# Kernel tuning notes

Hardware: AMD Instinct MI355X
Metric: run time of the kernel (lower is better)

## Reference

```python
import jax, jax.numpy as jnp
import numpy as np
from jax import lax

IN_C, OUT_C, K, Z_DIM, STRIDE = 128, 128, 3, 256, 1


def setup_inputs() -> dict:
    key = jax.random.key(0)
    k1, k2, k3, k4, k5 = jax.random.split(key, 5)
    B, H, W = 16, 64, 64
    x = jax.random.normal(k1, (B, IN_C, H, W), dtype=jnp.float32)
    z = jax.random.normal(k2, (B, Z_DIM), dtype=jnp.float32)
    # base conv weight, He-style init as in the torch module
    base_weight = jax.random.normal(k3, (OUT_C, IN_C, K, K), dtype=jnp.float32) * (2.0 / (IN_C * K * K)) ** 0.5
    # delta_weight_head: nn.Linear(z_dim, out_c*in_c*k*k) -> weight [out_dim, z_dim], bias [out_dim]
    out_dim = OUT_C * IN_C * K * K
    lim = 1.0 / np.sqrt(Z_DIM)
    head_w = jax.random.uniform(k4, (out_dim, Z_DIM), dtype=jnp.float32, minval=-lim, maxval=lim)
    head_b = jax.random.uniform(k5, (out_dim,), dtype=jnp.float32, minval=-lim, maxval=lim)
    return {"x": x, "z": z, "base_weight": base_weight, "head_w": head_w, "head_b": head_b}


def reference(x, z, base_weight, head_w, head_b):
    B = x.shape[0]
    # per-sample weight deltas: [B, out_c*in_c*k*k] -> [B, out_c, in_c, k, k]
    delta_w = (z @ head_w.T + head_b).reshape(B, OUT_C, IN_C, K, K)
    w = base_weight[None] + delta_w  # [B, out_c, in_c, k, k]
    pad = K // 2

    def conv_one(xb, wb):
        # xb: [in_c, H, W], wb: [out_c, in_c, k, k]
        return lax.conv_general_dilated(
            xb[None], wb, window_strides=(STRIDE, STRIDE),
            padding=[(pad, pad), (pad, pad)],
            dimension_numbers=("NCHW", "OIHW", "NCHW"))[0]

    out = jax.vmap(conv_one)(x, w)  # [B, out_c, H_out, W_out]
    return out
```

## Files before the change

### kernel.cpp

```cpp
#include <hip/hip_runtime.h>
#include <hip/hip_bf16.h>
#include <cstdint>
#include <cstddef>

typedef _Float16 f16;
typedef _Float16 f16x8 __attribute__((ext_vector_type(8)));
typedef _Float16 f16x4 __attribute__((ext_vector_type(4)));
typedef float f32x4 __attribute__((ext_vector_type(4)));

#define BATCH 16
#define INC   128
#define OUTC  128
#define HH    64
#define WW    64
#define HP    66
#define WP    66
#define ZDIM  256

#define XP_ELEMS (16ull * HP * WP * INC)
#define WA_ELEMS (16ull * 9 * OUTC * INC)

__global__ __launch_bounds__(256) void zero_xp(f16* __restrict__ xp) {
    unsigned i = blockIdx.x * 256 + threadIdx.x;
    unsigned b = i / 4160;
    unsigned j = i - b * 4160;
    unsigned row, wc, ic8;
    if (j < 2112) {
        row = (j < 1056) ? 0u : 65u;
        unsigned jj = (j < 1056) ? j : j - 1056;
        wc  = jj >> 4;
        ic8 = jj & 15;
    } else {
        unsigned j2 = j - 2112;
        row = 1 + (j2 >> 5);
        unsigned k = j2 & 31;
        wc  = (k < 16) ? 0u : 65u;
        ic8 = k & 15;
    }
    uint4 zv = {0u, 0u, 0u, 0u};
    *(uint4*)(xp + (((size_t)b * HP + row) * WP + wc) * INC + ic8 * 8) = zv;
}

__global__ __launch_bounds__(256) void xprep(const float* __restrict__ x,
                                             f16* __restrict__ xp) {
    int blk = blockIdx.x;
    int icC = blk & 3;
    int h   = (blk >> 2) & 63;
    int b   = blk >> 8;
    int ic0 = icC * 32;
    int tid = threadIdx.x;

    __shared__ float tile[32 * 65];

    {
        int i = tid >> 3;
        int j = tid & 7;
        const float4* src = (const float4*)(x + (((size_t)b * INC + ic0 + i) * HH + h) * WW) + j * 2;
        float4 v0 = src[0];
        float4 v1 = src[1];
        float* tp = tile + i * 65 + j * 8;
        tp[0] = v0.x; tp[1] = v0.y; tp[2] = v0.z; tp[3] = v0.w;
        tp[4] = v1.x; tp[5] = v1.y; tp[6] = v1.z; tp[7] = v1.w;
    }
    __syncthreads();
    {
        int w = tid >> 2;
        int q = tid & 3;
        f16 o8[8];
#pragma unroll
        for (int jj = 0; jj < 8; ++jj)
            o8[jj] = (f16)tile[(q * 8 + jj) * 65 + w];
        f16* dst = xp + (((size_t)b * HP + (h + 1)) * WP + (w + 1)) * INC + ic0 + q * 8;
        *(uint4*)dst = *(uint4*)o8;
    }
}

__device__ inline f16x8 cvt8(float4 a, float4 b) {
    f16x8 r;
    r[0] = (f16)a.x; r[1] = (f16)a.y; r[2] = (f16)a.z; r[3] = (f16)a.w;
    r[4] = (f16)b.x; r[5] = (f16)b.y; r[6] = (f16)b.z; r[7] = (f16)b.w;
    return r;
}

__global__ __launch_bounds__(256) void wgen(const float* __restrict__ z,
                                            const float* __restrict__ base_w,
                                            const float* __restrict__ head_w,
                                            const float* __restrict__ head_b,
                                            f16* __restrict__ wA) {
    int tid  = threadIdx.x;
    int lane = tid & 63;
    int wv   = tid >> 6;
    int r16  = lane & 15;
    int quad = lane >> 4;
    int tile = blockIdx.x * 4 + wv;
    int icb  = tile & 7;
    int oc   = (tile >> 3) & 127;
    int r    = tile >> 10;
    int base = (oc * 128 + icb * 16) * 9 + r;
    int myrow = base + 9 * r16;

    const float4* zrow = (const float4*)(z + (size_t)r16 * ZDIM);
    f16x8 bfr[8];
#pragma unroll
    for (int s = 0; s < 8; ++s)
        bfr[s] = cvt8(zrow[s * 8 + quad * 2], zrow[s * 8 + quad * 2 + 1]);

    const float4* hw = (const float4*)(head_w + (size_t)myrow * ZDIM);
    float4 a[3][2];
    a[0][0] = hw[quad * 2];     a[0][1] = hw[quad * 2 + 1];
    a[1][0] = hw[8 + quad * 2]; a[1][1] = hw[8 + quad * 2 + 1];
    f32x4 acc = {0.f, 0.f, 0.f, 0.f};
#pragma unroll
    for (int s = 0; s < 8; ++s) {
        if (s + 2 < 8) {
            a[(s + 2) % 3][0] = hw[(s + 2) * 8 + quad * 2];
            a[(s + 2) % 3][1] = hw[(s + 2) * 8 + quad * 2 + 1];
        }
        acc = __builtin_amdgcn_mfma_f32_16x16x32_f16(
            cvt8(a[s % 3][0], a[s % 3][1]), bfr[s], acc, 0, 0, 0);
    }

    f16x4 ov;
    int icl = quad * 4;
#pragma unroll
    for (int reg = 0; reg < 4; ++reg) {
        int o = base + 9 * (icl + reg);
        ov[reg] = (f16)(base_w[o] + head_b[o] + acc[reg]);
    }
    size_t idx = (((size_t)r16 * 9 + r) * OUTC + oc) * INC + icb * 16 + icl;
    *(f16x4*)(wA + idx) = ov;
}

__global__ __launch_bounds__(256) void conv(const f16* __restrict__ xp,
                                            const f16* __restrict__ wA,
                                            float* __restrict__ out) {
    int blk = blockIdx.x;
    int b  = blk >> 5;
    int pt = blk & 31;
    int h0 = pt * 2;

    int tid   = threadIdx.x;
    int lane  = tid & 63;
    int wv    = tid >> 6;
    int ocHalf = wv & 1;
    int pHalf  = wv >> 1;
    int m0    = ocHalf * 64;
    int row16 = lane & 15;
    int quad  = lane >> 4;

    __shared__ __align__(16) f16 ws3[3 * 128 * 40];
    __shared__ __align__(16) f16 xs[4 * 66 * 40];

    f32x4 acc[4][4];
#pragma unroll
    for (int mt = 0; mt < 4; ++mt)
#pragma unroll
        for (int nt = 0; nt < 4; ++nt)
            acc[mt][nt] = f32x4{0.f, 0.f, 0.f, 0.f};

    for (int c = 0; c < 4; ++c) {
        int ic0 = c * 32;
#pragma unroll
        for (int kh = 0; kh < 3; ++kh) {
            __syncthreads();
#pragma unroll
            for (int i = 0; i < 6; ++i) {
                int idx  = tid + i * 256;
                int seg  = idx >> 2;
                int part = idx & 3;
                int kw = seg >> 7;
                int oc = seg & 127;
                const uint4* src = (const uint4*)(wA +
                    ((((size_t)b * 9 + kh * 3 + kw) * OUTC + oc) * INC + ic0)) + part;
                *(uint4*)(ws3 + (kw * 128 + oc) * 40 + part * 8) = *src;
            }
            if (kh == 0) {
                for (int idx = tid; idx < 1056; idx += 256) {
                    int seg  = idx >> 2;
                    int part = idx & 3;
                    int row  = seg / 66;
                    int wc   = seg - row * 66;
                    const uint4* src = (const uint4*)(xp +
                        (((size_t)b * HP + h0 + row) * WP + wc) * INC + ic0) + part;
                    *(uint4*)(xs + (row * 66 + wc) * 40 + part * 8) = *src;
                }
            }
            __syncthreads();
#pragma unroll
            for (int kw = 0; kw < 3; ++kw) {
                f16x8 afr[4], bfr[4];
#pragma unroll
                for (int mt = 0; mt < 4; ++mt)
                    afr[mt] = *(const f16x8*)(ws3 + ((kw * 128 + m0 + mt * 16 + row16) * 40 + quad * 8));
#pragma unroll
                for (int nt = 0; nt < 4; ++nt)
                    bfr[nt] = *(const f16x8*)(xs + (((kh + pHalf) * 66 + nt * 16 + row16 + kw) * 40 + quad * 8));
#pragma unroll
                for (int mt = 0; mt < 4; ++mt)
#pragma unroll
                    for (int nt = 0; nt < 4; ++nt)
                        acc[mt][nt] = __builtin_amdgcn_mfma_f32_16x16x32_f16(
                            afr[mt], bfr[nt], acc[mt][nt], 0, 0, 0);
            }
        }
    }

    int hrow = h0 + pHalf;
#pragma unroll
    for (int mt = 0; mt < 4; ++mt)
#pragma unroll
        for (int nt = 0; nt < 4; ++nt) {
            int wc = nt * 16 + row16;
#pragma unroll
            for (int reg = 0; reg < 4; ++reg) {
                int oc = m0 + mt * 16 + quad * 4 + reg;
                out[(((size_t)b * OUTC + oc) * HH + hrow) * WW + wc] = acc[mt][nt][reg];
            }
        }
}

extern "C" void kernel_launch(void* const* d_in, const int* in_sizes, int n_in,
                              void* d_out, int out_size, void* d_ws, size_t ws_size,
                              hipStream_t stream) {
    const float* x      = (const float*)d_in[0];
    const float* z      = (const float*)d_in[1];
    const float* base_w = (const float*)d_in[2];
    const float* head_w = (const float*)d_in[3];
    const float* head_b = (const float*)d_in[4];
    float* out = (float*)d_out;

    f16* xp = (f16*)d_ws;
    f16* wAp = xp + XP_ELEMS;

    zero_xp<<<260, 256, 0, stream>>>(xp);
    xprep  <<<16 * 64 * 4, 256, 0, stream>>>(x, xp);
    wgen   <<<(OUTC * INC * 9) / 64, 256, 0, stream>>>(z, base_w, head_w,
                                                       head_b, wAp);
    conv   <<<16 * 32, 256, 0, stream>>>(xp, wAp, out);
}
```

Measured before the change: 288.8 us.

## Merge prep kernels and double-buffer conv weights via direct global-to-LDS loads

Folds the zero-padding, input transpose and weight-generation kernels into one launch, which removes two kernel launch gaps. In the conv kernel, weight tiles are double-buffered and fetched with global_load_lds so each next tile streams in while MFMAs run on the current one. Blocks are remapped so that batches are interleaved across XCDs, and the LDS row pitch drops from 40 to 32 halves. The unpadded pitch risks LDS bank conflicts, and the two-buffer scheme raises LDS use per block.

```diff
diff --git a/kernel.cpp b/kernel.cpp
--- a/kernel.cpp
+++ b/kernel.cpp
@@ -1,5 +1,4 @@
 #include <hip/hip_runtime.h>
-#include <hip/hip_bf16.h>
 #include <cstdint>
 #include <cstddef>
 
@@ -20,136 +19,143 @@
 #define XP_ELEMS (16ull * HP * WP * INC)
 #define WA_ELEMS (16ull * 9 * OUTC * INC)
 
-__global__ __launch_bounds__(256) void zero_xp(f16* __restrict__ xp) {
-    unsigned i = blockIdx.x * 256 + threadIdx.x;
-    unsigned b = i / 4160;
-    unsigned j = i - b * 4160;
-    unsigned row, wc, ic8;
-    if (j < 2112) {
-        row = (j < 1056) ? 0u : 65u;
-        unsigned jj = (j < 1056) ? j : j - 1056;
-        wc  = jj >> 4;
-        ic8 = jj & 15;
-    } else {
-        unsigned j2 = j - 2112;
-        row = 1 + (j2 >> 5);
-        unsigned k = j2 & 31;
-        wc  = (k < 16) ? 0u : 65u;
-        ic8 = k & 15;
-    }
-    uint4 zv = {0u, 0u, 0u, 0u};
-    *(uint4*)(xp + (((size_t)b * HP + row) * WP + wc) * INC + ic8 * 8) = zv;
-}
-
-__global__ __launch_bounds__(256) void xprep(const float* __restrict__ x,
-                                             f16* __restrict__ xp) {
-    int blk = blockIdx.x;
-    int icC = blk & 3;
-    int h   = (blk >> 2) & 63;
-    int b   = blk >> 8;
-    int ic0 = icC * 32;
-    int tid = threadIdx.x;
-
-    __shared__ float tile[32 * 65];
-
-    {
-        int i = tid >> 3;
-        int j = tid & 7;
-        const float4* src = (const float4*)(x + (((size_t)b * INC + ic0 + i) * HH + h) * WW) + j * 2;
-        float4 v0 = src[0];
-        float4 v1 = src[1];
-        float* tp = tile + i * 65 + j * 8;
-        tp[0] = v0.x; tp[1] = v0.y; tp[2] = v0.z; tp[3] = v0.w;
-        tp[4] = v1.x; tp[5] = v1.y; tp[6] = v1.z; tp[7] = v1.w;
-    }
-    __syncthreads();
-    {
-        int w = tid >> 2;
-        int q = tid & 3;
-        f16 o8[8];
-#pragma unroll
-        for (int jj = 0; jj < 8; ++jj)
-            o8[jj] = (f16)tile[(q * 8 + jj) * 65 + w];
-        f16* dst = xp + (((size_t)b * HP + (h + 1)) * WP + (w + 1)) * INC + ic0 + q * 8;
-        *(uint4*)dst = *(uint4*)o8;
-    }
-}
-
-__device__ inline f16x8 cvt8(float4 a, float4 b) {
+#define GLOAD16(g, l)                                                     \
+    __builtin_amdgcn_global_load_lds(                                     \
+        (const __attribute__((address_space(1))) void*)(g),               \
+        (__attribute__((address_space(3))) void*)(l), 16, 0, 0)
+
+__device__ __forceinline__ f16x8 cvt8(float4 a, float4 b) {
     f16x8 r;
     r[0] = (f16)a.x; r[1] = (f16)a.y; r[2] = (f16)a.z; r[3] = (f16)a.w;
     r[4] = (f16)b.x; r[5] = (f16)b.y; r[6] = (f16)b.z; r[7] = (f16)b.w;
     return r;
 }
 
-__global__ __launch_bounds__(256) void wgen(const float* __restrict__ z,
+__global__ __launch_bounds__(256) void prep(const float* __restrict__ x,
+                                            const float* __restrict__ z,
                                             const float* __restrict__ base_w,
                                             const float* __restrict__ head_w,
                                             const float* __restrict__ head_b,
+                                            f16* __restrict__ xp,
                                             f16* __restrict__ wA) {
-    int tid  = threadIdx.x;
-    int lane = tid & 63;
-    int wv   = tid >> 6;
-    int r16  = lane & 15;
-    int quad = lane >> 4;
-    int tile = blockIdx.x * 4 + wv;
-    int icb  = tile & 7;
-    int oc   = (tile >> 3) & 127;
-    int r    = tile >> 10;
-    int base = (oc * 128 + icb * 16) * 9 + r;
-    int myrow = base + 9 * r16;
-
-    const float4* zrow = (const float4*)(z + (size_t)r16 * ZDIM);
-    f16x8 bfr[8];
-#pragma unroll
-    for (int s = 0; s < 8; ++s)
-        bfr[s] = cvt8(zrow[s * 8 + quad * 2], zrow[s * 8 + quad * 2 + 1]);
-
-    const float4* hw = (const float4*)(head_w + (size_t)myrow * ZDIM);
-    float4 a[3][2];
-    a[0][0] = hw[quad * 2];     a[0][1] = hw[quad * 2 + 1];
-    a[1][0] = hw[8 + quad * 2]; a[1][1] = hw[8 + quad * 2 + 1];
-    f32x4 acc = {0.f, 0.f, 0.f, 0.f};
-#pragma unroll
-    for (int s = 0; s < 8; ++s) {
-        if (s + 2 < 8) {
-            a[(s + 2) % 3][0] = hw[(s + 2) * 8 + quad * 2];
-            a[(s + 2) % 3][1] = hw[(s + 2) * 8 + quad * 2 + 1];
-        }
-        acc = __builtin_amdgcn_mfma_f32_16x16x32_f16(
-            cvt8(a[s % 3][0], a[s % 3][1]), bfr[s], acc, 0, 0, 0);
+    __shared__ float tile[32 * 65];
+    int blk = blockIdx.x;
+    int tid = threadIdx.x;
+
+    if (blk < 2304) {
+        int lane = tid & 63;
+        int wv   = tid >> 6;
+        int r16  = lane & 15;
+        int quad = lane >> 4;
+        int tl   = blk * 4 + wv;
+        int icb  = tl & 7;
+        int oc   = (tl >> 3) & 127;
+        int r    = tl >> 10;
+        int base = (oc * 128 + icb * 16) * 9 + r;
+        int myrow = base + 9 * r16;
+
+        const float4* zrow = (const float4*)(z + (size_t)r16 * ZDIM);
+        f16x8 bfr[8];
+#pragma unroll
+        for (int s = 0; s < 8; ++s)
+            bfr[s] = cvt8(zrow[s * 8 + quad * 2], zrow[s * 8 + quad * 2 + 1]);
+
+        const float4* hw = (const float4*)(head_w + (size_t)myrow * ZDIM);
+        float4 a[3][2];
+        a[0][0] = hw[quad * 2];     a[0][1] = hw[quad * 2 + 1];
+        a[1][0] = hw[8 + quad * 2]; a[1][1] = hw[8 + quad * 2 + 1];
+        f32x4 acc = {0.f, 0.f, 0.f, 0.f};
+#pragma unroll
+        for (int s = 0; s < 8; ++s) {
+            if (s + 2 < 8) {
+                a[(s + 2) % 3][0] = hw[(s + 2) * 8 + quad * 2];
+                a[(s + 2) % 3][1] = hw[(s + 2) * 8 + quad * 2 + 1];
+            }
+            acc = __builtin_amdgcn_mfma_f32_16x16x32_f16(
+                cvt8(a[s % 3][0], a[s % 3][1]), bfr[s], acc, 0, 0, 0);
+        }
+
+        f16x4 ov;
+        int icl = quad * 4;
+#pragma unroll
+        for (int reg = 0; reg < 4; ++reg) {
+            int o = base + 9 * (icl + reg);
+            ov[reg] = (f16)(base_w[o] + head_b[o] + acc[reg]);
+        }
+        size_t idx = (((size_t)r16 * 9 + r) * OUTC + oc) * INC + icb * 16 + icl;
+        *(f16x4*)(wA + idx) = ov;
+
+    } else if (blk < 6400) {
+        int xb  = blk - 2304;
+        int icC = xb & 3;
+        int h   = (xb >> 2) & 63;
+        int b   = xb >> 8;
+        int ic0 = icC * 32;
+        {
+            int i = tid >> 3;
+            int j = tid & 7;
+            const float4* src = (const float4*)(x + (((size_t)b * INC + ic0 + i) * HH + h) * WW) + j * 2;
+            float4 v0 = src[0];
+            float4 v1 = src[1];
+            float* tp = tile + i * 65 + j * 8;
+            tp[0] = v0.x; tp[1] = v0.y; tp[2] = v0.z; tp[3] = v0.w;
+            tp[4] = v1.x; tp[5] = v1.y; tp[6] = v1.z; tp[7] = v1.w;
+        }
+        __syncthreads();
+        {
+            int w = tid >> 2;
+            int q = tid & 3;
+            f16 o8[8];
+#pragma unroll
+            for (int jj = 0; jj < 8; ++jj)
+                o8[jj] = (f16)tile[(q * 8 + jj) * 65 + w];
+            f16* dst = xp + (((size_t)b * HP + (h + 1)) * WP + (w + 1)) * INC + ic0 + q * 8;
+            *(uint4*)dst = *(uint4*)o8;
+        }
+
+    } else {
+        unsigned i = (unsigned)(blk - 6400) * 256u + (unsigned)tid;
+        unsigned b = i / 4160;
+        unsigned j = i - b * 4160;
+        unsigned row, wc, ic8;
+        if (j < 2112) {
+            row = (j < 1056) ? 0u : 65u;
+            unsigned jj = (j < 1056) ? j : j - 1056;
+            wc  = jj >> 4;
+            ic8 = jj & 15;
+        } else {
+            unsigned j2 = j - 2112;
+            row = 1 + (j2 >> 5);
+            unsigned k = j2 & 31;
+            wc  = (k < 16) ? 0u : 65u;
+            ic8 = k & 15;
+        }
+        uint4 zv = {0u, 0u, 0u, 0u};
+        *(uint4*)(xp + (((size_t)b * HP + row) * WP + wc) * INC + ic8 * 8) = zv;
     }
-
-    f16x4 ov;
-    int icl = quad * 4;
-#pragma unroll
-    for (int reg = 0; reg < 4; ++reg) {
-        int o = base + 9 * (icl + reg);
-        ov[reg] = (f16)(base_w[o] + head_b[o] + acc[reg]);
-    }
-    size_t idx = (((size_t)r16 * 9 + r) * OUTC + oc) * INC + icb * 16 + icl;
-    *(f16x4*)(wA + idx) = ov;
 }
 
 __global__ __launch_bounds__(256) void conv(const f16* __restrict__ xp,
                                             const f16* __restrict__ wA,
                                             float* __restrict__ out) {
-    int blk = blockIdx.x;
+    int blk0 = blockIdx.x;
+    int blk  = (blk0 & 7) * 64 + (blk0 >> 3);
     int b  = blk >> 5;
     int pt = blk & 31;
     int h0 = pt * 2;
 
-    int tid   = threadIdx.x;
-    int lane  = tid & 63;
-    int wv    = tid >> 6;
+    int tid    = threadIdx.x;
+    int lane   = tid & 63;
+    int wv     = tid >> 6;
     int ocHalf = wv & 1;
     int pHalf  = wv >> 1;
-    int m0    = ocHalf * 64;
-    int row16 = lane & 15;
-    int quad  = lane >> 4;
-
-    __shared__ __align__(16) f16 ws3[3 * 128 * 40];
-    __shared__ __align__(16) f16 xs[4 * 66 * 40];
+    int m0     = ocHalf * 64;
+    int row16  = lane & 15;
+    int quad   = lane >> 4;
+
+    __shared__ __align__(16) f16 ws0[3 * 128 * 32];
+    __shared__ __align__(16) f16 ws1[3 * 128 * 32];
+    __shared__ __align__(16) f16 xs [4 * 66 * 32];
 
     f32x4 acc[4][4];
 #pragma unroll
@@ -158,49 +164,71 @@
         for (int nt = 0; nt < 4; ++nt)
             acc[mt][nt] = f32x4{0.f, 0.f, 0.f, 0.f};
 
-    for (int c = 0; c < 4; ++c) {
-        int ic0 = c * 32;
-#pragma unroll
-        for (int kh = 0; kh < 3; ++kh) {
-            __syncthreads();
-#pragma unroll
-            for (int i = 0; i < 6; ++i) {
-                int idx  = tid + i * 256;
+    auto stage_w = [&](f16* wb, int c, int kh) {
+#pragma unroll
+        for (int i = 0; i < 6; ++i) {
+            int idx  = tid + i * 256;
+            int kw   = idx >> 9;
+            int oc   = (idx >> 2) & 127;
+            int part = idx & 3;
+            const f16* src = wA +
+                ((((size_t)b * 9 + kh * 3 + kw) * OUTC + oc) * INC + c * 32 + part * 8);
+            GLOAD16(src, wb + (size_t)idx * 8);
+        }
+    };
+    auto stage_x = [&](int c) {
+#pragma unroll
+        for (int i = 0; i < 5; ++i) {
+            int idx = tid + i * 256;
+            if (idx < 1056) {
                 int seg  = idx >> 2;
                 int part = idx & 3;
-                int kw = seg >> 7;
-                int oc = seg & 127;
-                const uint4* src = (const uint4*)(wA +
-                    ((((size_t)b * 9 + kh * 3 + kw) * OUTC + oc) * INC + ic0)) + part;
-                *(uint4*)(ws3 + (kw * 128 + oc) * 40 + part * 8) = *src;
-            }
-            if (kh == 0) {
-                for (int idx = tid; idx < 1056; idx += 256) {
-                    int seg  = idx >> 2;
-                    int part = idx & 3;
-                    int row  = seg / 66;
-                    int wc   = seg - row * 66;
-                    const uint4* src = (const uint4*)(xp +
-                        (((size_t)b * HP + h0 + row) * WP + wc) * INC + ic0) + part;
-                    *(uint4*)(xs + (row * 66 + wc) * 40 + part * 8) = *src;
-                }
-            }
-            __syncthreads();
+                int row  = seg / 66;
+                int wc   = seg - row * 66;
+                const f16* src = xp +
+                    ((((size_t)b * HP + h0 + row) * WP + wc) * INC + c * 32 + part * 8);
+                GLOAD16(src, xs + (size_t)idx * 8);
+            }
+        }
+    };
+
+    stage_x(0);
+    stage_w(ws0, 0, 0);
+    __syncthreads();
+
+#pragma unroll
+    for (int c = 0; c < 4; ++c) {
+#pragma unroll
+        for (int kh = 0; kh < 3; ++kh) {
+            const int s = c * 3 + kh;
+            f16* cur = (s & 1) ? ws1 : ws0;
+            if (s < 11) {
+                const int sn = s + 1;
+                f16* nxt = (sn & 1) ? ws1 : ws0;
+                stage_w(nxt, sn / 3, sn % 3);
+            }
 #pragma unroll
             for (int kw = 0; kw < 3; ++kw) {
                 f16x8 afr[4], bfr[4];
 #pragma unroll
                 for (int mt = 0; mt < 4; ++mt)
-                    afr[mt] = *(const f16x8*)(ws3 + ((kw * 128 + m0 + mt * 16 + row16) * 40 + quad * 8));
+                    afr[mt] = *(const f16x8*)(cur +
+                        ((size_t)(kw * 128 + m0 + mt * 16 + row16) * 32 + quad * 8));
 #pragma unroll
                 for (int nt = 0; nt < 4; ++nt)
-                    bfr[nt] = *(const f16x8*)(xs + (((kh + pHalf) * 66 + nt * 16 + row16 + kw) * 40 + quad * 8));
+                    bfr[nt] = *(const f16x8*)(xs +
+                        ((size_t)((kh + pHalf) * 66 + nt * 16 + row16 + kw) * 32 + quad * 8));
 #pragma unroll
                 for (int mt = 0; mt < 4; ++mt)
 #pragma unroll
                     for (int nt = 0; nt < 4; ++nt)
                         acc[mt][nt] = __builtin_amdgcn_mfma_f32_16x16x32_f16(
                             afr[mt], bfr[nt], acc[mt][nt], 0, 0, 0);
+            }
+            __syncthreads();
+            if (kh == 2 && c < 3) {
+                stage_x(c + 1);
+                __syncthreads();
             }
         }
     }
@@ -229,12 +257,9 @@
     const float* head_b = (const float*)d_in[4];
     float* out = (float*)d_out;
 
-    f16* xp = (f16*)d_ws;
+    f16* xp  = (f16*)d_ws;
     f16* wAp = xp + XP_ELEMS;
 
-    zero_xp<<<260, 256, 0, stream>>>(xp);
-    xprep  <<<16 * 64 * 4, 256, 0, stream>>>(x, xp);
-    wgen   <<<(OUTC * INC * 9) / 64, 256, 0, stream>>>(z, base_w, head_w,
-                                                       head_b, wAp);
-    conv   <<<16 * 32, 256, 0, stream>>>(xp, wAp, out);
-}
+    prep<<<6660, 256, 0, stream>>>(x, z, base_w, head_w, head_b, xp, wAp);
+    conv<<<512, 256, 0, stream>>>(xp, wAp, out);
+}
```

New measurement: 276.1 us. 1.05x faster.
